# Performance work log

Hardware: AMD Instinct MI355X
Metric: run time of the kernel (lower is better)

The kernel has to match this reference:

```python
import jax, jax.numpy as jnp
import numpy as np

NEG_SLOPE = 0.2
EPS = 1e-16  # matches PyG-style segment softmax denominator guard

N_NODES = 50000
N_EDGES = 800000
IN_CH = 256
HEADS = 4
OUT_CH = 32


def setup_inputs() -> dict:
    key = jax.random.key(0)
    k1, k2, k3, k4 = jax.random.split(key, 4)
    nodes_ft = jax.random.normal(k1, (N_NODES, IN_CH), dtype=jnp.float32)
    adj_list = jax.random.randint(k2, (2, N_EDGES), 0, N_NODES, dtype=jnp.int64)
    # xavier-normal-ish scales
    weight = jax.random.normal(k3, (IN_CH, HEADS * OUT_CH), dtype=jnp.float32) * (
        (2.0 / (IN_CH + HEADS * OUT_CH)) ** 0.5
    )
    att = jax.random.normal(k4, (1, HEADS, 2 * OUT_CH), dtype=jnp.float32) * (
        (2.0 / (1 + 2 * OUT_CH)) ** 0.5
    )
    bias = jnp.zeros((HEADS * OUT_CH,), dtype=jnp.float32)
    return {"nodes_ft": nodes_ft, "adj_list": adj_list, "weight": weight, "att": att, "bias": bias}


def reference(nodes_ft, adj_list, weight, att, bias):
    N = nodes_ft.shape[0]
    H, C = att.shape[1], att.shape[2] // 2
    dst = adj_list[0]  # softmax / aggregation key
    src = adj_list[1]
    # node hidden states: [N, H, C]
    h = (nodes_ft @ weight).reshape(N, H, C)
    xi = h[dst]  # [E, H, C]
    xj = h[src]  # [E, H, C]
    # attention logits: cat([xi, xj]) . att  ==  xi.att_i + xj.att_j
    att_i, att_j = att[:, :, :C], att[:, :, C:]
    alpha = (xi * att_i).sum(-1) + (xj * att_j).sum(-1)  # [E, H]
    alpha = jax.nn.leaky_relu(alpha, negative_slope=NEG_SLOPE)
    # segment softmax over destination node
    m = jax.ops.segment_max(alpha, dst, num_segments=N)  # [N, H]
    m = jnp.where(jnp.isfinite(m), m, 0.0)
    e = jnp.exp(alpha - m[dst])
    s = jax.ops.segment_sum(e, dst, num_segments=N)  # [N, H]
    a = e / (s[dst] + EPS)  # [E, H]
    # weighted scatter-add aggregate
    vals = xj * a[:, :, None]  # [E, H, C]
    out = jax.ops.segment_sum(vals, dst, num_segments=N)  # [N, H, C]
    out = out.reshape(N, H * C) + bias  # concat=True
    return out
```

## Files before the change

### kernel.cpp

```cpp
#include <hip/hip_runtime.h>
#include <hip/hip_bf16.h>
#include <math.h>

#define NN 50000
#define NE 800000
#define IN_CH 256
#define HEADS 4
#define OUT_CH 32
#define HC 128
#define NEG_SLOPE 0.2f
#define GAT_EPS 1e-16f

#define SBS 1024
#define NB  ((NN + SBS - 1) / SBS)

#define NBINS 64
#define BINSH 10
#define NBBIN 49
#define NBLK  625
#define EPB   1280

#define OFF_HB     0
#define OFF_WT     (NN*HC/2)
#define OFF_AI     (OFF_WT + 16384)
#define OFF_AJ     (OFF_AI + NN*HEADS)
#define OFF_ROW    (OFF_AJ + NN*HEADS)
#define OFF_CUR    (OFF_ROW + NN + 4)
#define OFF_HIST   (OFF_CUR + NN + 4)
#define OFF_BSUM   (OFF_HIST + NN + 4)
#define OFF_BOFF   (OFF_BSUM + NB + 4)
#define OFF_BLKC   (OFF_BOFF + NB + 4)
#define OFF_BLKO   (OFF_BLKC + NBLK*NBINS)
#define OFF_PAIR   ((OFF_BLKO + NBLK*NBINS + 1) & ~1)
#define OFF_ESRC   (OFF_PAIR + 2*NE)

typedef __attribute__((ext_vector_type(8))) short short8v;
typedef __attribute__((ext_vector_type(4))) float float4v;

__device__ __forceinline__ unsigned short f2bf(float x) {
    union { float f; unsigned u; } v; v.f = x;
    unsigned r = v.u + 0x7fffu + ((v.u >> 16) & 1u);
    return (unsigned short)(r >> 16);
}
__device__ __forceinline__ float bf2f(unsigned short b) {
    union { unsigned u; float f; } v; v.u = ((unsigned)b) << 16;
    return v.f;
}

__global__ void k_zero(int* __restrict__ hist) {
    int i = blockIdx.x * blockDim.x + threadIdx.x;
    if (i < NN) hist[i] = 0;
}

__global__ void k_wt(const float* __restrict__ W, unsigned short* __restrict__ Wt) {
    int idx = blockIdx.x * blockDim.x + threadIdx.x;
    if (idx >= HC * IN_CH) return;
    int n = idx >> 8, k = idx & 255;
    Wt[n * IN_CH + k] = f2bf(W[(size_t)k * HC + n]);
}

__global__ __launch_bounds__(256) void k_gemm(const float* __restrict__ A,
                                              const unsigned short* __restrict__ Wt,
                                              unsigned short* __restrict__ Hb) {
    const int tid  = threadIdx.x;
    const int lane = tid & 63;
    const int w    = tid >> 6;
    const int wr   = w >> 1, wc = w & 1;
    const int blockRow = blockIdx.x * 128;

    const int lrow = lane & 15;
    const int kgrp = lane >> 4;

    float4v acc[4][4];
#pragma unroll
    for (int i = 0; i < 4; i++)
#pragma unroll
        for (int j = 0; j < 4; j++) acc[i][j] = (float4v){0.f, 0.f, 0.f, 0.f};

#pragma unroll
    for (int ks = 0; ks < 8; ks++) {
        const int kb = ks * 32 + kgrp * 8;
        short8v af[4], bfr[4];
#pragma unroll
        for (int mi = 0; mi < 4; mi++) {
            int r = blockRow + wr * 64 + mi * 16 + lrow;
            if (r >= NN) r = NN - 1;
            const float* ap = A + (size_t)r * IN_CH + kb;
            float4 a0 = *(const float4*)ap;
            float4 a1 = *(const float4*)(ap + 4);
            short8v t;
            t[0] = (short)f2bf(a0.x); t[1] = (short)f2bf(a0.y);
            t[2] = (short)f2bf(a0.z); t[3] = (short)f2bf(a0.w);
            t[4] = (short)f2bf(a1.x); t[5] = (short)f2bf(a1.y);
            t[6] = (short)f2bf(a1.z); t[7] = (short)f2bf(a1.w);
            af[mi] = t;
        }
#pragma unroll
        for (int ni = 0; ni < 4; ni++) {
            int c = wc * 64 + ni * 16 + lrow;
            bfr[ni] = *(const short8v*)(Wt + (size_t)c * IN_CH + kb);
        }
#pragma unroll
        for (int mi = 0; mi < 4; mi++)
#pragma unroll
            for (int ni = 0; ni < 4; ni++)
                acc[mi][ni] = __builtin_amdgcn_mfma_f32_16x16x32_bf16(
                    af[mi], bfr[ni], acc[mi][ni], 0, 0, 0);
    }

#pragma unroll
    for (int mi = 0; mi < 4; mi++) {
#pragma unroll
        for (int reg = 0; reg < 4; reg++) {
            int r = blockRow + wr * 64 + mi * 16 + kgrp * 4 + reg;
            if (r >= NN) continue;
#pragma unroll
            for (int ni = 0; ni < 4; ni++) {
                int c = wc * 64 + ni * 16 + lrow;
                Hb[(size_t)r * HC + c] = f2bf(acc[mi][ni][reg]);
            }
        }
    }
}

__global__ void k_att(const unsigned short* __restrict__ Hb, const float* __restrict__ att,
                      float* __restrict__ ai, float* __restrict__ aj) {
    int idx = blockIdx.x * blockDim.x + threadIdx.x;
    if (idx >= NN * HEADS) return;
    int n = idx >> 2, hh = idx & 3;
    const unsigned* hp = (const unsigned*)(Hb + (size_t)n * HC + hh * OUT_CH);
    const float* ati = att + hh * 2 * OUT_CH;
    const float* atj = ati + OUT_CH;
    float si = 0.f, sj = 0.f;
#pragma unroll
    for (int i = 0; i < 16; i++) {
        unsigned u = hp[i];
        float lo = bf2f((unsigned short)(u & 0xffff));
        float hi = bf2f((unsigned short)(u >> 16));
        si = fmaf(lo, ati[2 * i], si);     si = fmaf(hi, ati[2 * i + 1], si);
        sj = fmaf(lo, atj[2 * i], sj);     sj = fmaf(hi, atj[2 * i + 1], sj);
    }
    ai[idx] = si;
    aj[idx] = sj;
}

__global__ __launch_bounds__(256) void s_count(const int* __restrict__ adj,
                                               int* __restrict__ hist,
                                               int* __restrict__ blkcnt) {
    __shared__ int lh[NBINS];
    int b = blockIdx.x, t = threadIdx.x;
    if (t < NBINS) lh[t] = 0;
    __syncthreads();
    int e0 = b * EPB;
#pragma unroll
    for (int i = 0; i < 5; i++) {
        int e = e0 + i * 256 + t;
        int dst = adj[e];
        atomicAdd(&hist[dst], 1);
        atomicAdd(&lh[dst >> BINSH], 1);
    }
    __syncthreads();
    if (t < NBINS) blkcnt[b * NBINS + t] = lh[t];
}

__global__ __launch_bounds__(640) void s_scanblk(const int* __restrict__ blkcnt,
                                                 int* __restrict__ blkoff) {
    int bin = blockIdx.x, t = threadIdx.x;
    int c = (t < NBLK) ? blkcnt[t * NBINS + bin] : 0;
    int lane = t & 63, w = t >> 6;
    int inc = c;
#pragma unroll
    for (int off = 1; off < 64; off <<= 1) {
        int u = __shfl_up(inc, off);
        if (lane >= off) inc += u;
    }
    __shared__ int wsum[10];
    if (lane == 63) wsum[w] = inc;
    __syncthreads();
    int wpre = 0;
    for (int i = 0; i < w; i++) wpre += wsum[i];
    if (t < NBLK) blkoff[t * NBINS + bin] = wpre + inc - c;
}

__global__ __launch_bounds__(256) void s_pairs(const int* __restrict__ adj,
                                               const int* __restrict__ rowp,
                                               const int* __restrict__ blkoff,
                                               int2* __restrict__ paired) {
    __shared__ int lh[NBINS];
    __shared__ int base[NBINS];
    int b = blockIdx.x, t = threadIdx.x;
    if (t < NBINS) {
        lh[t] = 0;
        int n0 = t << BINSH;
        base[t] = rowp[n0 < NN ? n0 : NN] + blkoff[b * NBINS + t];
    }
    __syncthreads();
    int e0 = b * EPB;
#pragma unroll
    for (int i = 0; i < 5; i++) {
        int e = e0 + i * 256 + t;
        int dst = adj[e];
        int src = adj[NE + e];
        int bin = dst >> BINSH;
        int r = atomicAdd(&lh[bin], 1);
        paired[base[bin] + r] = make_int2(dst, src);
    }
}

__global__ __launch_bounds__(256) void s_csr(const int2* __restrict__ paired,
                                             const int* __restrict__ rowp,
                                             int* __restrict__ esrc) {
    __shared__ int cur2[1 << BINSH];
    int b = blockIdx.x, t = threadIdx.x;
    for (int i = t; i < (1 << BINSH); i += 256) cur2[i] = 0;
    __syncthreads();
    int n0 = b << BINSH;
    int n1 = n0 + (1 << BINSH); if (n1 > NN) n1 = NN;
    int e0 = rowp[n0], e1 = rowp[n1];
    for (int i = e0 + t; i < e1; i += 256) {
        int2 p = paired[i];
        int off = atomicAdd(&cur2[p.x - n0], 1);
        esrc[rowp[p.x] + off] = p.y;
    }
}

__global__ __launch_bounds__(256) void k_bsum(const int* __restrict__ hist,
                                              int* __restrict__ bsum) {
    int b = blockIdx.x, t = threadIdx.x;
    int i0 = b * SBS + t * 4;
    int s = 0;
#pragma unroll
    for (int j = 0; j < 4; j++) {
        int i = i0 + j;
        if (i < NN) s += hist[i];
    }
#pragma unroll
    for (int off = 32; off; off >>= 1) s += __shfl_xor(s, off);
    __shared__ int ws[4];
    int lane = t & 63, wid = t >> 6;
    if (lane == 0) ws[wid] = s;
    __syncthreads();
    if (t == 0) bsum[b] = ws[0] + ws[1] + ws[2] + ws[3];
}

__global__ __launch_bounds__(64) void k_bscan(const int* __restrict__ bsum,
                                              int* __restrict__ boff) {
    int lane = threadIdx.x;
    int v = (lane < NB) ? bsum[lane] : 0;
    int inc = v;
#pragma unroll
    for (int off = 1; off < 64; off <<= 1) {
        int u = __shfl_up(inc, off);
        if (lane >= off) inc += u;
    }
    if (lane < NB) boff[lane] = inc - v;
}

__global__ __launch_bounds__(256) void k_bwrite(const int* __restrict__ hist,
                                                const int* __restrict__ boff,
                                                int* __restrict__ row,
                                                int* __restrict__ cur) {
    int b = blockIdx.x, t = threadIdx.x;
    int i0 = b * SBS + t * 4;
    int v[4];
    int s = 0;
#pragma unroll
    for (int j = 0; j < 4; j++) {
        int i = i0 + j;
        v[j] = (i < NN) ? hist[i] : 0;
        s += v[j];
    }
    int lane = t & 63, wid = t >> 6;
    int inc = s;
#pragma unroll
    for (int off = 1; off < 64; off <<= 1) {
        int u = __shfl_up(inc, off);
        if (lane >= off) inc += u;
    }
    __shared__ int wsum[4];
    if (lane == 63) wsum[wid] = inc;
    __syncthreads();
    int woff = 0;
    for (int w2 = 0; w2 < wid; w2++) woff += wsum[w2];
    int run = boff[b] + woff + (inc - s);
#pragma unroll
    for (int j = 0; j < 4; j++) {
        int i = i0 + j;
        if (i < NN) {
            row[i] = run;
            cur[i] = run;
            run += v[j];
        }
    }
    if (b == 0 && t == 0) row[NN] = NE;
}

__device__ __forceinline__ float lrelu(float x) {
    return x > 0.f ? x : NEG_SLOPE * x;
}

__global__ __launch_bounds__(256) void k_gather(const int* __restrict__ row,
                                                const int* __restrict__ esrc,
                                                const float* __restrict__ ai,
                                                const float* __restrict__ aj,
                                                const unsigned short* __restrict__ Hb,
                                                const float* __restrict__ bias,
                                                float* __restrict__ out) {
    int gid = blockIdx.x * blockDim.x + threadIdx.x;
    int nid = gid >> 6;
    int lane = gid & 63;
    if (nid >= NN) return;
    int r0 = row[nid];
    int deg = row[nid + 1] - r0;

    float4 aiv = *(const float4*)&ai[nid * 4];

    float mx0 = -INFINITY, mx1 = -INFINITY, mx2 = -INFINITY, mx3 = -INFINITY;
    for (int k = lane; k < deg; k += 64) {
        int s = esrc[r0 + k];
        float4 ajv = *(const float4*)&aj[s * 4];
        mx0 = fmaxf(mx0, lrelu(aiv.x + ajv.x));
        mx1 = fmaxf(mx1, lrelu(aiv.y + ajv.y));
        mx2 = fmaxf(mx2, lrelu(aiv.z + ajv.z));
        mx3 = fmaxf(mx3, lrelu(aiv.w + ajv.w));
    }
#pragma unroll
    for (int off = 32; off; off >>= 1) {
        mx0 = fmaxf(mx0, __shfl_xor(mx0, off));
        mx1 = fmaxf(mx1, __shfl_xor(mx1, off));
        mx2 = fmaxf(mx2, __shfl_xor(mx2, off));
        mx3 = fmaxf(mx3, __shfl_xor(mx3, off));
    }

    float s0 = 0.f, s1 = 0.f, s2 = 0.f, s3 = 0.f;
    for (int k = lane; k < deg; k += 64) {
        int s = esrc[r0 + k];
        float4 ajv = *(const float4*)&aj[s * 4];
        s0 += __expf(lrelu(aiv.x + ajv.x) - mx0);
        s1 += __expf(lrelu(aiv.y + ajv.y) - mx1);
        s2 += __expf(lrelu(aiv.z + ajv.z) - mx2);
        s3 += __expf(lrelu(aiv.w + ajv.w) - mx3);
    }
#pragma unroll
    for (int off = 32; off; off >>= 1) {
        s0 += __shfl_xor(s0, off);
        s1 += __shfl_xor(s1, off);
        s2 += __shfl_xor(s2, off);
        s3 += __shfl_xor(s3, off);
    }

    int c0 = lane * 2;
    int hh = lane >> 4;
    float mh  = (hh & 2) ? ((hh & 1) ? mx3 : mx2) : ((hh & 1) ? mx1 : mx0);
    float sh  = (hh & 2) ? ((hh & 1) ? s3 : s2) : ((hh & 1) ? s1 : s0);
    float aih = (hh & 2) ? ((hh & 1) ? aiv.w : aiv.z) : ((hh & 1) ? aiv.y : aiv.x);
    float inv = 1.0f / (sh + GAT_EPS);

    float accx = 0.f, accy = 0.f;
#pragma unroll 4
    for (int k = 0; k < deg; k++) {
        int s = esrc[r0 + k];
        float al = lrelu(aih + aj[s * 4 + hh]);
        float a = __expf(al - mh) * inv;
        unsigned hu = *(const unsigned*)(Hb + (size_t)s * HC + c0);
        accx = fmaf(bf2f((unsigned short)(hu & 0xffff)), a, accx);
        accy = fmaf(bf2f((unsigned short)(hu >> 16)), a, accy);
    }
    out[(size_t)nid * HC + c0]     = accx + bias[c0];
    out[(size_t)nid * HC + c0 + 1] = accy + bias[c0 + 1];
}

extern "C" void kernel_launch(void* const* d_in, const int* in_sizes, int n_in,
                              void* d_out, int out_size, void* d_ws, size_t ws_size,
                              hipStream_t stream) {
    const float* nodes  = (const float*)d_in[0];
    const int*   adj    = (const int*)d_in[1];
    const float* weight = (const float*)d_in[2];
    const float* att    = (const float*)d_in[3];
    const float* bias   = (const float*)d_in[4];
    float* out = (float*)d_out;
    float* ws  = (float*)d_ws;

    unsigned short* Hb = (unsigned short*)(ws + OFF_HB);
    unsigned short* Wt = (unsigned short*)(ws + OFF_WT);
    float* ai    = ws + OFF_AI;
    float* aj    = ws + OFF_AJ;
    int*   rowp  = (int*)(ws + OFF_ROW);
    int*   cur   = (int*)(ws + OFF_CUR);
    int*   hist  = (int*)(ws + OFF_HIST);
    int*   bsum  = (int*)(ws + OFF_BSUM);
    int*   boff  = (int*)(ws + OFF_BOFF);
    int*   blkc  = (int*)(ws + OFF_BLKC);
    int*   blko  = (int*)(ws + OFF_BLKO);
    int2*  pair  = (int2*)(ws + OFF_PAIR);
    int*   esrc  = (int*)(ws + OFF_ESRC);

    k_zero<<<(NN + 255) / 256, 256, 0, stream>>>(hist);
    s_count<<<NBLK, 256, 0, stream>>>(adj, hist, blkc);
    k_bsum<<<NB, 256, 0, stream>>>(hist, bsum);
    k_bscan<<<1, 64, 0, stream>>>(bsum, boff);
    k_bwrite<<<NB, 256, 0, stream>>>(hist, boff, rowp, cur);
    s_scanblk<<<NBINS, 640, 0, stream>>>(blkc, blko);
    s_pairs<<<NBLK, 256, 0, stream>>>(adj, rowp, blko, pair);
    s_csr<<<NBBIN, 256, 0, stream>>>(pair, rowp, esrc);
    k_wt<<<(HC * IN_CH + 255) / 256, 256, 0, stream>>>(weight, Wt);
    k_gemm<<<(NN + 127) / 128, 256, 0, stream>>>(nodes, Wt, Hb);
    k_att<<<(NN * HEADS + 255) / 256, 256, 0, stream>>>(Hb, att, ai, aj);
    k_gather<<<(NN * 64 + 255) / 256, 256, 0, stream>>>(rowp, esrc, ai, aj, Hb, bias, out);
}
```

Measured before the change: 275.2 us.

## Fuse softmax sum into aggregation, merge init kernels, inline block scan

The gather kernel drops the separate pass that computed the softmax denominator. It now accumulates the exp sum together with the weighted features, with two edges in flight per wave (half-wave per edge, 4 channels per lane), and normalizes once at the end. The zeroing and weight-transpose kernels are merged into one launch. The block-offset scan kernel is folded into k_bwrite, and the unused cur array write is removed. This cuts kernel launches and one pass over neighbor attention values, at the cost of lanes idling when an edge pair is incomplete and a serial loop over edges that is half as long.

```diff
diff --git a/kernel.cpp b/kernel.cpp
--- a/kernel.cpp
+++ b/kernel.cpp
@@ -25,11 +25,9 @@
 #define OFF_AI     (OFF_WT + 16384)
 #define OFF_AJ     (OFF_AI + NN*HEADS)
 #define OFF_ROW    (OFF_AJ + NN*HEADS)
-#define OFF_CUR    (OFF_ROW + NN + 4)
-#define OFF_HIST   (OFF_CUR + NN + 4)
+#define OFF_HIST   (OFF_ROW + NN + 4)
 #define OFF_BSUM   (OFF_HIST + NN + 4)
-#define OFF_BOFF   (OFF_BSUM + NB + 4)
-#define OFF_BLKC   (OFF_BOFF + NB + 4)
+#define OFF_BLKC   (OFF_BSUM + NB + 4)
 #define OFF_BLKO   (OFF_BLKC + NBLK*NBINS)
 #define OFF_PAIR   ((OFF_BLKO + NBLK*NBINS + 1) & ~1)
 #define OFF_ESRC   (OFF_PAIR + 2*NE)
@@ -42,21 +40,23 @@
     unsigned r = v.u + 0x7fffu + ((v.u >> 16) & 1u);
     return (unsigned short)(r >> 16);
 }
-__device__ __forceinline__ float bf2f(unsigned short b) {
-    union { unsigned u; float f; } v; v.u = ((unsigned)b) << 16;
+__device__ __forceinline__ float bf2f_lo(unsigned u) {
+    union { unsigned u; float f; } v; v.u = u << 16;
     return v.f;
 }
-
-__global__ void k_zero(int* __restrict__ hist) {
-    int i = blockIdx.x * blockDim.x + threadIdx.x;
-    if (i < NN) hist[i] = 0;
-}
-
-__global__ void k_wt(const float* __restrict__ W, unsigned short* __restrict__ Wt) {
+__device__ __forceinline__ float bf2f_hi(unsigned u) {
+    union { unsigned u; float f; } v; v.u = u & 0xffff0000u;
+    return v.f;
+}
+
+__global__ void k_init(int* __restrict__ hist, const float* __restrict__ W,
+                       unsigned short* __restrict__ Wt) {
     int idx = blockIdx.x * blockDim.x + threadIdx.x;
-    if (idx >= HC * IN_CH) return;
-    int n = idx >> 8, k = idx & 255;
-    Wt[n * IN_CH + k] = f2bf(W[(size_t)k * HC + n]);
+    if (idx < NN) hist[idx] = 0;
+    if (idx < HC * IN_CH) {
+        int n = idx >> 8, k = idx & 255;
+        Wt[n * IN_CH + k] = f2bf(W[(size_t)k * HC + n]);
+    }
 }
 
 __global__ __launch_bounds__(256) void k_gemm(const float* __restrict__ A,
@@ -135,8 +135,8 @@
 #pragma unroll
     for (int i = 0; i < 16; i++) {
         unsigned u = hp[i];
-        float lo = bf2f((unsigned short)(u & 0xffff));
-        float hi = bf2f((unsigned short)(u >> 16));
+        float lo = bf2f_lo(u);
+        float hi = bf2f_hi(u);
         si = fmaf(lo, ati[2 * i], si);     si = fmaf(hi, ati[2 * i + 1], si);
         sj = fmaf(lo, atj[2 * i], sj);     sj = fmaf(hi, atj[2 * i + 1], sj);
     }
@@ -243,24 +243,18 @@
     if (t == 0) bsum[b] = ws[0] + ws[1] + ws[2] + ws[3];
 }
 
-__global__ __launch_bounds__(64) void k_bscan(const int* __restrict__ bsum,
-                                              int* __restrict__ boff) {
-    int lane = threadIdx.x;
-    int v = (lane < NB) ? bsum[lane] : 0;
-    int inc = v;
-#pragma unroll
-    for (int off = 1; off < 64; off <<= 1) {
-        int u = __shfl_up(inc, off);
-        if (lane >= off) inc += u;
-    }
-    if (lane < NB) boff[lane] = inc - v;
-}
-
 __global__ __launch_bounds__(256) void k_bwrite(const int* __restrict__ hist,
-                                                const int* __restrict__ boff,
-                                                int* __restrict__ row,
-                                                int* __restrict__ cur) {
+                                                const int* __restrict__ bsum,
+                                                int* __restrict__ row) {
+    __shared__ int s_boff;
     int b = blockIdx.x, t = threadIdx.x;
+    if (t < 64) {
+        int v = (t < b) ? bsum[t] : 0;
+#pragma unroll
+        for (int off = 32; off; off >>= 1) v += __shfl_xor(v, off);
+        if (t == 0) s_boff = v;
+    }
+    __syncthreads();
     int i0 = b * SBS + t * 4;
     int v[4];
     int s = 0;
@@ -282,13 +276,12 @@
     __syncthreads();
     int woff = 0;
     for (int w2 = 0; w2 < wid; w2++) woff += wsum[w2];
-    int run = boff[b] + woff + (inc - s);
+    int run = s_boff + woff + (inc - s);
 #pragma unroll
     for (int j = 0; j < 4; j++) {
         int i = i0 + j;
         if (i < NN) {
             row[i] = run;
-            cur[i] = run;
             run += v[j];
         }
     }
@@ -332,42 +325,46 @@
         mx3 = fmaxf(mx3, __shfl_xor(mx3, off));
     }
 
-    float s0 = 0.f, s1 = 0.f, s2 = 0.f, s3 = 0.f;
-    for (int k = lane; k < deg; k += 64) {
-        int s = esrc[r0 + k];
-        float4 ajv = *(const float4*)&aj[s * 4];
-        s0 += __expf(lrelu(aiv.x + ajv.x) - mx0);
-        s1 += __expf(lrelu(aiv.y + ajv.y) - mx1);
-        s2 += __expf(lrelu(aiv.z + ajv.z) - mx2);
-        s3 += __expf(lrelu(aiv.w + ajv.w) - mx3);
-    }
-#pragma unroll
-    for (int off = 32; off; off >>= 1) {
-        s0 += __shfl_xor(s0, off);
-        s1 += __shfl_xor(s1, off);
-        s2 += __shfl_xor(s2, off);
-        s3 += __shfl_xor(s3, off);
-    }
-
-    int c0 = lane * 2;
-    int hh = lane >> 4;
+    int cl = lane & 31;
+    int c0 = cl * 4;
+    int hh = cl >> 3;
     float mh  = (hh & 2) ? ((hh & 1) ? mx3 : mx2) : ((hh & 1) ? mx1 : mx0);
-    float sh  = (hh & 2) ? ((hh & 1) ? s3 : s2) : ((hh & 1) ? s1 : s0);
     float aih = (hh & 2) ? ((hh & 1) ? aiv.w : aiv.z) : ((hh & 1) ? aiv.y : aiv.x);
-    float inv = 1.0f / (sh + GAT_EPS);
-
-    float accx = 0.f, accy = 0.f;
-#pragma unroll 4
-    for (int k = 0; k < deg; k++) {
-        int s = esrc[r0 + k];
-        float al = lrelu(aih + aj[s * 4 + hh]);
-        float a = __expf(al - mh) * inv;
-        unsigned hu = *(const unsigned*)(Hb + (size_t)s * HC + c0);
-        accx = fmaf(bf2f((unsigned short)(hu & 0xffff)), a, accx);
-        accy = fmaf(bf2f((unsigned short)(hu >> 16)), a, accy);
-    }
-    out[(size_t)nid * HC + c0]     = accx + bias[c0];
-    out[(size_t)nid * HC + c0 + 1] = accy + bias[c0 + 1];
+
+    float ax = 0.f, ay = 0.f, az = 0.f, aw = 0.f;
+    float asum = 0.f;
+    int ec2 = lane >> 5;
+    for (int kc = 0; kc < deg; kc += 2) {
+        int k = kc + ec2;
+        int s = 0;
+        float av = 0.f;
+        if (k < deg) {
+            s = esrc[r0 + k];
+            av = __expf(lrelu(aih + aj[s * 4 + hh]) - mh);
+        }
+        asum += av;
+        uint2 hu = *(const uint2*)(Hb + (size_t)s * HC + c0);
+        ax = fmaf(bf2f_lo(hu.x), av, ax);
+        ay = fmaf(bf2f_hi(hu.x), av, ay);
+        az = fmaf(bf2f_lo(hu.y), av, az);
+        aw = fmaf(bf2f_hi(hu.y), av, aw);
+    }
+    ax += __shfl_xor(ax, 32);
+    ay += __shfl_xor(ay, 32);
+    az += __shfl_xor(az, 32);
+    aw += __shfl_xor(aw, 32);
+    asum += __shfl_xor(asum, 32);
+
+    if (lane < 32) {
+        float inv = 1.0f / (asum + GAT_EPS);
+        float4 bv = *(const float4*)&bias[c0];
+        float4 o;
+        o.x = fmaf(ax, inv, bv.x);
+        o.y = fmaf(ay, inv, bv.y);
+        o.z = fmaf(az, inv, bv.z);
+        o.w = fmaf(aw, inv, bv.w);
+        *(float4*)&out[(size_t)nid * HC + c0] = o;
+    }
 }
 
 extern "C" void kernel_launch(void* const* d_in, const int* in_sizes, int n_in,
@@ -386,24 +383,20 @@
     float* ai    = ws + OFF_AI;
     float* aj    = ws + OFF_AJ;
     int*   rowp  = (int*)(ws + OFF_ROW);
-    int*   cur   = (int*)(ws + OFF_CUR);
     int*   hist  = (int*)(ws + OFF_HIST);
     int*   bsum  = (int*)(ws + OFF_BSUM);
-    int*   boff  = (int*)(ws + OFF_BOFF);
     int*   blkc  = (int*)(ws + OFF_BLKC);
     int*   blko  = (int*)(ws + OFF_BLKO);
     int2*  pair  = (int2*)(ws + OFF_PAIR);
     int*   esrc  = (int*)(ws + OFF_ESRC);
 
-    k_zero<<<(NN + 255) / 256, 256, 0, stream>>>(hist);
+    k_init<<<(NN + 255) / 256, 256, 0, stream>>>(hist, weight, Wt);
     s_count<<<NBLK, 256, 0, stream>>>(adj, hist, blkc);
     k_bsum<<<NB, 256, 0, stream>>>(hist, bsum);
-    k_bscan<<<1, 64, 0, stream>>>(bsum, boff);
-    k_bwrite<<<NB, 256, 0, stream>>>(hist, boff, rowp, cur);
+    k_bwrite<<<NB, 256, 0, stream>>>(hist, bsum, rowp);
     s_scanblk<<<NBINS, 640, 0, stream>>>(blkc, blko);
     s_pairs<<<NBLK, 256, 0, stream>>>(adj, rowp, blko, pair);
     s_csr<<<NBBIN, 256, 0, stream>>>(pair, rowp, esrc);
-    k_wt<<<(HC * IN_CH + 255) / 256, 256, 0, stream>>>(weight, Wt);
     k_gemm<<<(NN + 127) / 128, 256, 0, stream>>>(nodes, Wt, Hb);
     k_att<<<(NN * HEADS + 255) / 256, 256, 0, stream>>>(Hb, att, ai, aj);
     k_gather<<<(NN * 64 + 255) / 256, 256, 0, stream>>>(rowp, esrc, ai, aj, Hb, bias, out);
```

Result: slower. 288.2 us (+4.7%).
